# Kernel optimization log

Measured on AMD Instinct MI355X. Metric: run time of the kernel, lower is better.

The kernel has to match this reference:

```python
import jax, jax.numpy as jnp
import numpy as np

OUTPUT_BIT = 8
N_SCALE = 28          # scale_bits
EXP_BITS = 16
SEGMENTS = 16
DEGREE = 2
S_VAL = 0.03          # input quantization scale


def _fit_pieces(s):
    # Mirrors _compute_integer_coefficients for backend='float':
    # fit exp((x_off-127)*s) over offset domain x_off*s in [-128s, 127s].
    xs_off = np.linspace(-128.0, 127.0, 10000)
    ys = np.exp((xs_off - 127.0) * s)
    xs = xs_off * s
    bounds = np.linspace(-128.0 * s, 127.0 * s, SEGMENTS + 1)
    coeffs = np.zeros((SEGMENTS, DEGREE + 1))  # ascending powers a0,a1,a2
    for j in range(SEGMENTS):
        m = (xs >= bounds[j]) & (xs <= bounds[j + 1])
        coeffs[j] = np.polyfit(xs[m], ys[m], DEGREE)[::-1]
    # integer coefficients: p(x_int*s)*2^N = sum_k floor(a_k*s^k*2^N)*x_int^k
    pw = s ** np.arange(DEGREE + 1)
    coeffs_int = np.floor(coeffs * pw[None, :] * (2.0 ** N_SCALE))
    lo_int = np.floor(bounds[:-1] / s)  # integer segment lower bounds
    return lo_int.astype(np.float32), coeffs_int.astype(np.float32)


def setup_inputs() -> dict:
    key = jax.random.key(0)
    x = jax.random.normal(key, (8, 12, 512, 512), dtype=jnp.float32) * 4.0
    scaling_factor = jnp.full((1,), S_VAL, dtype=jnp.float32)
    lo_np, cf_np = _fit_pieces(S_VAL)
    return {
        "x": x,
        "scaling_factor": scaling_factor,
        "lo_bounds": jnp.asarray(lo_np),
        "coeffs": jnp.asarray(cf_np),
    }


def floor_ste(y):
    # floor with straight-through gradient
    return y + jax.lax.stop_gradient(jnp.floor(y) - y)


def reference(x, scaling_factor, lo_bounds, coeffs):
    s = scaling_factor
    x_int = floor_ste(x / s)
    x_int = x_int - jnp.max(x_int, axis=-1, keepdims=True) + 127.0

    # piecewise-polynomial integer exp (computed under no_grad in the original)
    xi = jax.lax.stop_gradient(x_int)
    idx = jnp.clip(jnp.searchsorted(lo_bounds, xi, side="right") - 1, 0, SEGMENTS - 1)
    c = coeffs[idx]                         # [..., deg+1], ascending powers
    r = c[..., DEGREE]
    for k in range(DEGREE - 1, -1, -1):     # Horner evaluation
        r = r * xi + c[..., k]
    exp_int = jnp.maximum(jax.lax.stop_gradient(r), 0.0)

    exp_int = floor_ste(exp_int / 2.0 ** (30 - EXP_BITS + 1))
    exp_sum = jnp.maximum(jnp.sum(exp_int, axis=-1, keepdims=True), 1.0)
    factor = jnp.floor(2.0 ** 32 / jax.lax.stop_gradient(exp_sum))
    softmax_int = jnp.floor(jax.lax.stop_gradient(exp_int) * factor / 2.0 ** (32 - OUTPUT_BIT + 1))

    softmax_float = jax.nn.softmax(x, axis=-1)
    s_out = jnp.array([2.0 / 2 ** OUTPUT_BIT], dtype=x.dtype)
    smi_f = softmax_int * s_out
    # STE: integer value forward, float-softmax gradient backward
    output = jax.lax.stop_gradient(smi_f) + (softmax_float - jax.lax.stop_gradient(softmax_float))
    output = s_out * floor_ste(output / s_out)
    return output, s_out
```

## Files before the change

kernel.cpp:

```cpp
#include <hip/hip_runtime.h>


#define ROWLEN 512

typedef float nfloat4 __attribute__((ext_vector_type(4)));

#define DPP_SUM_I32(t)                                                        \
    t += __builtin_amdgcn_update_dpp(0, t, 0x111, 0xf, 0xf, true);            \
    t += __builtin_amdgcn_update_dpp(0, t, 0x112, 0xf, 0xf, true);            \
    t += __builtin_amdgcn_update_dpp(0, t, 0x114, 0xf, 0xf, true);            \
    t += __builtin_amdgcn_update_dpp(0, t, 0x118, 0xf, 0xf, true);            \
    t += __builtin_amdgcn_update_dpp(0, t, 0x142, 0xa, 0xf, true);            \
    t += __builtin_amdgcn_update_dpp(0, t, 0x143, 0xc, 0xf, true);

#define DPP_MAX_F32_STEP(m, ctrl, rmask)                                      \
    {                                                                         \
        int _mi = __float_as_int(m);                                          \
        int _sh = __builtin_amdgcn_update_dpp(_mi, _mi, ctrl, rmask, 0xf, false); \
        m = fmaxf(m, __int_as_float(_sh));                                    \
    }
#define DPP_MIN_F32_STEP(m, ctrl, rmask)                                      \
    {                                                                         \
        int _mi = __float_as_int(m);                                          \
        int _sh = __builtin_amdgcn_update_dpp(_mi, _mi, ctrl, rmask, 0xf, false); \
        m = fminf(m, __int_as_float(_sh));                                    \
    }

__global__ __launch_bounds__(256, 8) void ppis_kernel(
    const float* __restrict__ x,
    const float* __restrict__ sfp,
    const float* __restrict__ lo,
    const float* __restrict__ cf,
    float* __restrict__ out,
    int nrows)
{
    __shared__ int  s_e[1024];
    __shared__ int4 s_cf[16];

    const int tid  = threadIdx.x;
    const int lane = tid & 63;
    const int wid  = tid >> 6;

    const long long row = (long long)blockIdx.x * 4 + wid;
    const float4* xp = reinterpret_cast<const float4*>(x) + row * (ROWLEN / 4);
    const float4 va = xp[lane];
    const float4 vb = xp[lane + 64];

    const float s  = sfp[0];
    const float ry = 1.0f / s;

    if (tid < 16)
        s_cf[tid] = make_int4((int)cf[tid*3+0], (int)cf[tid*3+1], (int)cf[tid*3+2], 0);

    {
        int4 ev;
        int* evp = reinterpret_cast<int*>(&ev);
        const int j0 = tid * 4;
        #pragma unroll
        for (int jj = 0; jj < 4; ++jj) {
            const int j  = j0 + jj;
            const int u  = j - 768;
            const int uc = u < 0 ? 0 : u;
            int idx = ((uc + 1) * 257) >> 12;
            idx = idx > 15 ? 15 : idx;
            const int c0 = (int)cf[idx * 3 + 0];
            const int c1 = (int)cf[idx * 3 + 1];
            const int c2 = (int)cf[idx * 3 + 2];
            const int xi = j - 896;
            const int r1 = c2 * xi + c1;
            long long r2 = (long long)r1 * xi + c0;
            if (r2 < 0) r2 = 0;
            evp[jj] = (int)(r2 >> 15);
        }
        reinterpret_cast<int4*>(s_e)[tid] = ev;
    }
    __syncthreads();

    const float xv[8] = {va.x, va.y, va.z, va.w, vb.x, vb.y, vb.z, vb.w};

    float mf = fmaxf(fmaxf(fmaxf(xv[0], xv[1]), fmaxf(xv[2], xv[3])),
                     fmaxf(fmaxf(xv[4], xv[5]), fmaxf(xv[6], xv[7])));
    float nf_ = fminf(fminf(fminf(xv[0], xv[1]), fminf(xv[2], xv[3])),
                      fminf(fminf(xv[4], xv[5]), fminf(xv[6], xv[7])));
    DPP_MAX_F32_STEP(mf, 0x111, 0xf)  DPP_MIN_F32_STEP(nf_, 0x111, 0xf)
    DPP_MAX_F32_STEP(mf, 0x112, 0xf)  DPP_MIN_F32_STEP(nf_, 0x112, 0xf)
    DPP_MAX_F32_STEP(mf, 0x114, 0xf)  DPP_MIN_F32_STEP(nf_, 0x114, 0xf)
    DPP_MAX_F32_STEP(mf, 0x118, 0xf)  DPP_MIN_F32_STEP(nf_, 0x118, 0xf)
    DPP_MAX_F32_STEP(mf, 0x142, 0xa)  DPP_MIN_F32_STEP(nf_, 0x142, 0xa)
    DPP_MAX_F32_STEP(mf, 0x143, 0xc)  DPP_MIN_F32_STEP(nf_, 0x143, 0xc)
    const float xmax = __int_as_float(__builtin_amdgcn_readlane(__float_as_int(mf), 63));
    const float xmin = __int_as_float(__builtin_amdgcn_readlane(__float_as_int(nf_), 63));

    auto fdiv_floor = [&](float xk) -> int {
        float nf = floorf(xk * ry);
        const float d = fmaf(-s, nf, xk);
        nf = (d < 0.0f) ? nf - 1.0f : nf;
        const float u = fmaf(-s, nf + 1.0f, xk);
        nf = (u >= 0.0f) ? nf + 1.0f : nf;
        return (int)nf;
    };

    int n[8];
    #pragma unroll
    for (int k = 0; k < 8; ++k) n[k] = fdiv_floor(xv[k]);
    const int mx = fdiv_floor(xmax);
    const int mn = fdiv_floor(xmin);

    const int joff = 1023 - mx;

    int e[8];
    int tsum = 0;
    if (mn + joff >= 0) {
        #pragma unroll
        for (int k = 0; k < 8; ++k) {
            e[k] = s_e[n[k] + joff];
            tsum += e[k];
        }
    } else {
        #pragma unroll
        for (int k = 0; k < 8; ++k) {
            const int u  = n[k] + (255 - mx);
            const int uc = u < 0 ? 0 : u;
            int idx = ((uc + 1) * 257) >> 12;
            idx = idx > 15 ? 15 : idx;
            const int4 c = s_cf[idx];
            const long long xi = (long long)(u - 128);
            long long r2 = ((long long)c.z * xi + c.y) * xi + c.x;
            if (r2 < 0) r2 = 0;
            e[k] = (int)(r2 >> 15);
            tsum += e[k];
        }
    }

    DPP_SUM_I32(tsum)
    int ts = __builtin_amdgcn_readlane(tsum, 63);
    if (ts < 1) ts = 1;

    const unsigned int factor =
        (unsigned int)floor(__ddiv_rn(4294967296.0, (double)ts));

    nfloat4 o0, o1;
    #pragma unroll
    for (int k = 0; k < 4; ++k) {
        const unsigned long long p0 = (unsigned long long)(unsigned int)e[k]   * factor;
        const unsigned long long p1 = (unsigned long long)(unsigned int)e[k+4] * factor;
        o0[k] = (float)(int)(p0 >> 25) * 0.0078125f;
        o1[k] = (float)(int)(p1 >> 25) * 0.0078125f;
    }

    nfloat4* op = reinterpret_cast<nfloat4*>(out) + row * (ROWLEN / 4);
    __builtin_nontemporal_store(o0, op + lane);
    __builtin_nontemporal_store(o1, op + lane + 64);

    if (row == 0 && lane == 0)
        out[(long long)nrows * ROWLEN] = 0.0078125f;
}

extern "C" void kernel_launch(void* const* d_in, const int* in_sizes, int n_in,
                              void* d_out, int out_size, void* d_ws, size_t ws_size,
                              hipStream_t stream) {
    const float* x  = (const float*)d_in[0];
    const float* sf = (const float*)d_in[1];
    const float* lo = (const float*)d_in[2];
    const float* cf = (const float*)d_in[3];
    float* out = (float*)d_out;

    const int nrows = in_sizes[0] / ROWLEN;
    ppis_kernel<<<nrows / 4, 256, 0, stream>>>(x, sf, lo, cf, out, nrows);
}
```

Measured before the change: 181.1 us.

## Use persistent grid-stride blocks with next-row prefetch and integer max reduction

The launch now uses a capped persistent grid of 2048 blocks. Each block loops over row groups and prefetches the next group's inputs while computing the current one, and the shared exp table is built once per block instead of once per 4 rows. The max reduction now runs on the floored integers rather than on floats with a separate min pass, and the 64-bit multiply-shift becomes a single umulhi. The catch is fewer blocks, so less latency hiding from occupancy, and more registers per thread for the prefetch.

```diff
diff --git a/kernel.cpp b/kernel.cpp
--- a/kernel.cpp
+++ b/kernel.cpp
@@ -13,17 +13,10 @@
     t += __builtin_amdgcn_update_dpp(0, t, 0x142, 0xa, 0xf, true);            \
     t += __builtin_amdgcn_update_dpp(0, t, 0x143, 0xc, 0xf, true);
 
-#define DPP_MAX_F32_STEP(m, ctrl, rmask)                                      \
+#define DPP_MAX_I32_STEP(m, ctrl, rmask)                                      \
     {                                                                         \
-        int _mi = __float_as_int(m);                                          \
-        int _sh = __builtin_amdgcn_update_dpp(_mi, _mi, ctrl, rmask, 0xf, false); \
-        m = fmaxf(m, __int_as_float(_sh));                                    \
-    }
-#define DPP_MIN_F32_STEP(m, ctrl, rmask)                                      \
-    {                                                                         \
-        int _mi = __float_as_int(m);                                          \
-        int _sh = __builtin_amdgcn_update_dpp(_mi, _mi, ctrl, rmask, 0xf, false); \
-        m = fminf(m, __int_as_float(_sh));                                    \
+        int _sh = __builtin_amdgcn_update_dpp(m, m, ctrl, rmask, 0xf, false); \
+        m = (_sh > m) ? _sh : m;                                              \
     }
 
 __global__ __launch_bounds__(256, 8) void ppis_kernel(
@@ -34,23 +27,24 @@
     float* __restrict__ out,
     int nrows)
 {
-    __shared__ int  s_e[1024];
-    __shared__ int4 s_cf[16];
+    __shared__ int s_e[1024];
 
     const int tid  = threadIdx.x;
     const int lane = tid & 63;
     const int wid  = tid >> 6;
 
-    const long long row = (long long)blockIdx.x * 4 + wid;
-    const float4* xp = reinterpret_cast<const float4*>(x) + row * (ROWLEN / 4);
-    const float4 va = xp[lane];
-    const float4 vb = xp[lane + 64];
+    const long long ngroups = (long long)(nrows >> 2);
+    const long long gstride = gridDim.x;
+
+    long long grp = blockIdx.x;
+
+    const float4* xb = reinterpret_cast<const float4*>(x);
+    const float4* xp = xb + (grp * 4 + wid) * (ROWLEN / 4);
+    float4 va = xp[lane];
+    float4 vb = xp[lane + 64];
 
     const float s  = sfp[0];
     const float ry = 1.0f / s;
-
-    if (tid < 16)
-        s_cf[tid] = make_int4((int)cf[tid*3+0], (int)cf[tid*3+1], (int)cf[tid*3+2], 0);
 
     {
         int4 ev;
@@ -76,84 +70,108 @@
     }
     __syncthreads();
 
-    const float xv[8] = {va.x, va.y, va.z, va.w, vb.x, vb.y, vb.z, vb.w};
+    nfloat4* ob = reinterpret_cast<nfloat4*>(out);
 
-    float mf = fmaxf(fmaxf(fmaxf(xv[0], xv[1]), fmaxf(xv[2], xv[3])),
-                     fmaxf(fmaxf(xv[4], xv[5]), fmaxf(xv[6], xv[7])));
-    float nf_ = fminf(fminf(fminf(xv[0], xv[1]), fminf(xv[2], xv[3])),
-                      fminf(fminf(xv[4], xv[5]), fminf(xv[6], xv[7])));
-    DPP_MAX_F32_STEP(mf, 0x111, 0xf)  DPP_MIN_F32_STEP(nf_, 0x111, 0xf)
-    DPP_MAX_F32_STEP(mf, 0x112, 0xf)  DPP_MIN_F32_STEP(nf_, 0x112, 0xf)
-    DPP_MAX_F32_STEP(mf, 0x114, 0xf)  DPP_MIN_F32_STEP(nf_, 0x114, 0xf)
-    DPP_MAX_F32_STEP(mf, 0x118, 0xf)  DPP_MIN_F32_STEP(nf_, 0x118, 0xf)
-    DPP_MAX_F32_STEP(mf, 0x142, 0xa)  DPP_MIN_F32_STEP(nf_, 0x142, 0xa)
-    DPP_MAX_F32_STEP(mf, 0x143, 0xc)  DPP_MIN_F32_STEP(nf_, 0x143, 0xc)
-    const float xmax = __int_as_float(__builtin_amdgcn_readlane(__float_as_int(mf), 63));
-    const float xmin = __int_as_float(__builtin_amdgcn_readlane(__float_as_int(nf_), 63));
+    while (true) {
+        const long long nxt = grp + gstride;
+        const bool more = (nxt < ngroups);
+        float4 va2, vb2;
+        if (more) {
+            const float4* xq = xb + (nxt * 4 + wid) * (ROWLEN / 4);
+            va2 = xq[lane];
+            vb2 = xq[lane + 64];
+        }
 
-    auto fdiv_floor = [&](float xk) -> int {
-        float nf = floorf(xk * ry);
-        const float d = fmaf(-s, nf, xk);
-        nf = (d < 0.0f) ? nf - 1.0f : nf;
-        const float u = fmaf(-s, nf + 1.0f, xk);
-        nf = (u >= 0.0f) ? nf + 1.0f : nf;
-        return (int)nf;
-    };
+        const float xv[8] = {va.x, va.y, va.z, va.w, vb.x, vb.y, vb.z, vb.w};
 
-    int n[8];
-    #pragma unroll
-    for (int k = 0; k < 8; ++k) n[k] = fdiv_floor(xv[k]);
-    const int mx = fdiv_floor(xmax);
-    const int mn = fdiv_floor(xmin);
+        auto fdiv_floor = [&](float xk) -> int {
+            float nf = floorf(xk * ry);
+            const float d = fmaf(-s, nf, xk);
+            nf = (d < 0.0f) ? nf - 1.0f : nf;
+            const float u = fmaf(-s, nf + 1.0f, xk);
+            nf = (u >= 0.0f) ? nf + 1.0f : nf;
+            return (int)nf;
+        };
 
-    const int joff = 1023 - mx;
+        int n[8];
+        #pragma unroll
+        for (int k = 0; k < 8; ++k) n[k] = fdiv_floor(xv[k]);
 
-    int e[8];
-    int tsum = 0;
-    if (mn + joff >= 0) {
+        int ml = n[0];
         #pragma unroll
-        for (int k = 0; k < 8; ++k) {
-            e[k] = s_e[n[k] + joff];
-            tsum += e[k];
+        for (int k = 1; k < 8; ++k) ml = (n[k] > ml) ? n[k] : ml;
+        DPP_MAX_I32_STEP(ml, 0x111, 0xf)
+        DPP_MAX_I32_STEP(ml, 0x112, 0xf)
+        DPP_MAX_I32_STEP(ml, 0x114, 0xf)
+        DPP_MAX_I32_STEP(ml, 0x118, 0xf)
+        DPP_MAX_I32_STEP(ml, 0x142, 0xa)
+        DPP_MAX_I32_STEP(ml, 0x143, 0xc)
+        const int mx = __builtin_amdgcn_readlane(ml, 63);
+
+        const int joff = 1023 - mx;
+
+        int jm;
+        {
+            #pragma unroll
+            for (int k = 0; k < 8; ++k) n[k] += joff;
+            jm = n[0];
+            #pragma unroll
+            for (int k = 1; k < 8; ++k) jm = (n[k] < jm) ? n[k] : jm;
         }
-    } else {
+
+        int e[8];
+        int tsum = 0;
+        if (!__any(jm < 0)) {
+            #pragma unroll
+            for (int k = 0; k < 8; ++k) {
+                e[k] = s_e[n[k]];
+                tsum += e[k];
+            }
+        } else {
+            #pragma unroll 1
+            for (int k = 0; k < 8; ++k) {
+                const int u  = n[k] - 768;
+                const int uc = u < 0 ? 0 : u;
+                int idx = ((uc + 1) * 257) >> 12;
+                idx = idx > 15 ? 15 : idx;
+                const long long c0 = (long long)(int)cf[idx * 3 + 0];
+                const long long c1 = (long long)(int)cf[idx * 3 + 1];
+                const long long c2 = (long long)(int)cf[idx * 3 + 2];
+                const long long xi = (long long)(n[k] - 896);
+                long long r2 = (c2 * xi + c1) * xi + c0;
+                if (r2 < 0) r2 = 0;
+                e[k] = (int)(r2 >> 15);
+                tsum += e[k];
+            }
+        }
+
+        DPP_SUM_I32(tsum)
+        int ts = __builtin_amdgcn_readlane(tsum, 63);
+        if (ts < 1) ts = 1;
+
+        const unsigned int factor =
+            (unsigned int)floor(__ddiv_rn(4294967296.0, (double)ts));
+        const unsigned int f7 = factor << 7;
+
+        nfloat4 o0, o1;
         #pragma unroll
-        for (int k = 0; k < 8; ++k) {
-            const int u  = n[k] + (255 - mx);
-            const int uc = u < 0 ? 0 : u;
-            int idx = ((uc + 1) * 257) >> 12;
-            idx = idx > 15 ? 15 : idx;
-            const int4 c = s_cf[idx];
-            const long long xi = (long long)(u - 128);
-            long long r2 = ((long long)c.z * xi + c.y) * xi + c.x;
-            if (r2 < 0) r2 = 0;
-            e[k] = (int)(r2 >> 15);
-            tsum += e[k];
+        for (int k = 0; k < 4; ++k) {
+            o0[k] = (float)__umulhi((unsigned int)e[k],     f7) * 0.0078125f;
+            o1[k] = (float)__umulhi((unsigned int)e[k + 4], f7) * 0.0078125f;
         }
+
+        nfloat4* op = ob + (grp * 4 + wid) * (ROWLEN / 4);
+        __builtin_nontemporal_store(o0, op + lane);
+        __builtin_nontemporal_store(o1, op + lane + 64);
+
+        if (grp == 0 && wid == 0 && lane == 0)
+            out[(long long)nrows * ROWLEN] = 0.0078125f;
+
+        if (!more) break;
+        grp = nxt;
+        va  = va2;
+        vb  = vb2;
     }
-
-    DPP_SUM_I32(tsum)
-    int ts = __builtin_amdgcn_readlane(tsum, 63);
-    if (ts < 1) ts = 1;
-
-    const unsigned int factor =
-        (unsigned int)floor(__ddiv_rn(4294967296.0, (double)ts));
-
-    nfloat4 o0, o1;
-    #pragma unroll
-    for (int k = 0; k < 4; ++k) {
-        const unsigned long long p0 = (unsigned long long)(unsigned int)e[k]   * factor;
-        const unsigned long long p1 = (unsigned long long)(unsigned int)e[k+4] * factor;
-        o0[k] = (float)(int)(p0 >> 25) * 0.0078125f;
-        o1[k] = (float)(int)(p1 >> 25) * 0.0078125f;
-    }
-
-    nfloat4* op = reinterpret_cast<nfloat4*>(out) + row * (ROWLEN / 4);
-    __builtin_nontemporal_store(o0, op + lane);
-    __builtin_nontemporal_store(o1, op + lane + 64);
-
-    if (row == 0 && lane == 0)
-        out[(long long)nrows * ROWLEN] = 0.0078125f;
 }
 
 extern "C" void kernel_launch(void* const* d_in, const int* in_sizes, int n_in,
@@ -165,6 +183,8 @@
     const float* cf = (const float*)d_in[3];
     float* out = (float*)d_out;
 
-    const int nrows = in_sizes[0] / ROWLEN;
-    ppis_kernel<<<nrows / 4, 256, 0, stream>>>(x, sf, lo, cf, out, nrows);
+    const int nrows   = in_sizes[0] / ROWLEN;
+    const int ngroups = nrows / 4;
+    const int grid    = ngroups < 2048 ? ngroups : 2048;
+    ppis_kernel<<<grid, 256, 0, stream>>>(x, sf, lo, cf, out, nrows);
 }
```

Measured after the change: 186.2 us. 2.8% more time.
